# Optimization experiments

Hardware: AMD Instinct MI355X
Metric: run time of the kernel (lower is better)

The kernel has to match this reference:

```python
import jax, jax.numpy as jnp
import numpy as np

FEAT_STRIDE = 16
NMS_THRESH = 0.7
N_PRE = 6000    # eval-mode n_test_pre_nms
N_POST = 300    # eval-mode n_test_post_nms
MIN_SIZE = 16.0
NEG = -1e9
N_ANCHOR = 9


def generate_anchor_base():
    base = 16.0
    ratios = np.array([0.5, 1.0, 2.0], dtype=np.float64)
    scales = np.array([8.0, 16.0, 32.0], dtype=np.float64)
    h = (base * scales[None, :] * np.sqrt(ratios[:, None])).reshape(-1)
    w = (base * scales[None, :] * np.sqrt(1.0 / ratios[:, None])).reshape(-1)
    yc = xc = base / 2.0
    ab = np.stack([yc - h / 2, xc - w / 2, yc + h / 2, xc + w / 2], axis=1)
    return ab.astype(np.float32)  # [9,4] (y1,x1,y2,x2)


def enumerate_anchors(hh, ww):
    ab = generate_anchor_base()                       # [A,4]
    sy = np.arange(hh) * FEAT_STRIDE
    sx = np.arange(ww) * FEAT_STRIDE
    sx, sy = np.meshgrid(sx, sy)
    shift = np.stack([sy.ravel(), sx.ravel(), sy.ravel(), sx.ravel()], axis=1)  # [K,4]
    anchor = (shift[:, None, :] + ab[None, :, :]).reshape(-1, 4)                # [K*A,4]
    return jnp.asarray(anchor.astype(np.float32))


def conv2d(x, w, b, pad):
    y = jax.lax.conv_general_dilated(
        x, w, window_strides=(1, 1), padding=[(pad, pad), (pad, pad)],
        dimension_numbers=('NCHW', 'OIHW', 'NCHW'))
    return y + b[None, :, None, None]


def loc2bbox(anchor, loc):
    # anchor, loc: [K,4]; boxes as (y1,x1,y2,x2), deltas as (dy,dx,dh,dw)
    h = anchor[:, 2] - anchor[:, 0]
    w = anchor[:, 3] - anchor[:, 1]
    yc = anchor[:, 0] + 0.5 * h
    xc = anchor[:, 1] + 0.5 * w
    cy = loc[:, 0] * h + yc
    cx = loc[:, 1] * w + xc
    nh = jnp.exp(loc[:, 2]) * h
    nw = jnp.exp(loc[:, 3]) * w
    return jnp.stack([cy - 0.5 * nh, cx - 0.5 * nw, cy + 0.5 * nh, cx + 0.5 * nw], axis=1)


def iou_matrix(b):
    # b: [N,4] -> [N,N] pairwise IoU (same convention as torchvision.ops.nms)
    area = (b[:, 2] - b[:, 0]) * (b[:, 3] - b[:, 1])
    tl = jnp.maximum(b[:, None, :2], b[None, :, :2])
    br = jnp.minimum(b[:, None, 2:], b[None, :, 2:])
    wh = jnp.clip(br - tl, 0.0)
    inter = wh[..., 0] * wh[..., 1]
    return inter / (area[:, None] + area[None, :] - inter + 1e-9)


def propose(loc, score, anchor, img_h, img_w):
    # loc: [K,4] float, score: [K] fg prob, anchor: [K,4]
    roi = loc2bbox(anchor, loc)
    roi = jnp.stack([
        jnp.clip(roi[:, 0], 0.0, img_h), jnp.clip(roi[:, 1], 0.0, img_w),
        jnp.clip(roi[:, 2], 0.0, img_h), jnp.clip(roi[:, 3], 0.0, img_w)], axis=1)
    hs = roi[:, 2] - roi[:, 0]
    ws = roi[:, 3] - roi[:, 1]
    valid = (hs >= MIN_SIZE) & (ws >= MIN_SIZE)
    score = jnp.where(valid, score, NEG)        # filter-by-size via score masking
    vals, idx = jax.lax.top_k(score, N_PRE)      # descending score sort + pre-NMS cut
    boxes = roi[idx]                             # [N_PRE,4]
    iou = iou_matrix(boxes)
    supp0 = vals <= NEG / 2                      # filtered boxes start suppressed
    ar = jnp.arange(N_PRE)

    def body(i, supp):
        row = (iou[i] > NMS_THRESH) & (ar > i)
        return jnp.where(supp[i], supp, supp | row)

    supp = jax.lax.fori_loop(0, N_PRE, body, supp0)
    keep = ~supp
    kept = jnp.nonzero(keep, size=N_POST, fill_value=0)[0]
    n_keep = jnp.sum(keep)
    valid_out = jnp.arange(N_POST) < n_keep
    rois = jnp.where(valid_out[:, None], boxes[kept], 0.0)  # zero-padded [N_POST,4]
    return rois


def rpn_forward(x, conv1_w, conv1_b, score_w, score_b, loc_w, loc_b, img_h, img_w):
    n, _, hh, ww = x.shape
    anchor = enumerate_anchors(hh, ww)                        # [K*A,4]
    hidden = jax.nn.relu(conv2d(x, conv1_w, conv1_b, 1))      # [n,512,hh,ww]
    rpn_locs = conv2d(hidden, loc_w, loc_b, 0)                # [n,36,hh,ww]
    rpn_locs = rpn_locs.transpose(0, 2, 3, 1).reshape(n, -1, 4)
    raw = conv2d(hidden, score_w, score_b, 0).transpose(0, 2, 3, 1)  # [n,hh,ww,18]
    sm = jax.nn.softmax(raw.reshape(n, hh, ww, N_ANCHOR, 2), axis=4)
    fg = sm[..., 1].reshape(n, -1)                            # [n, K*A]
    rpn_scores = raw.reshape(n, -1, 2)
    rois = jax.vmap(lambda l, s: propose(l, s, anchor, float(img_h), float(img_w)))(rpn_locs, fg)
    roi_indices = jnp.repeat(jnp.arange(n, dtype=jnp.int32), N_POST)
    return rpn_locs, rpn_scores, rois.reshape(-1, 4), roi_indices, anchor


def setup_inputs() -> dict:
    key = jax.random.key(0)
    ks = jax.random.split(key, 7)
    n, c, hh, ww = 2, 512, 50, 84
    mid = 512
    x = jax.random.normal(ks[0], (n, c, hh, ww), dtype=jnp.float32)
    conv1_w = 0.01 * jax.random.normal(ks[1], (mid, c, 3, 3), dtype=jnp.float32)
    conv1_b = jnp.zeros((mid,), dtype=jnp.float32)
    score_w = 0.01 * jax.random.normal(ks[2], (N_ANCHOR * 2, mid, 1, 1), dtype=jnp.float32)
    score_b = jnp.zeros((N_ANCHOR * 2,), dtype=jnp.float32)
    loc_w = 0.01 * jax.random.normal(ks[3], (N_ANCHOR * 4, mid, 1, 1), dtype=jnp.float32)
    loc_b = jnp.zeros((N_ANCHOR * 4,), dtype=jnp.float32)
    return {"x": x, "conv1_w": conv1_w, "conv1_b": conv1_b,
            "score_w": score_w, "score_b": score_b,
            "loc_w": loc_w, "loc_b": loc_b,
            "img_h": 800, "img_w": 1344}


def reference(x, conv1_w, conv1_b, score_w, score_b, loc_w, loc_b, img_h, img_w):
    return rpn_forward(x, conv1_w, conv1_b, score_w, score_b, loc_w, loc_b, img_h, img_w)
```

## Files before the change

### kernel.cpp

```cpp
#include <hip/hip_runtime.h>
#include <hip/hip_bf16.h>
#include <math.h>

#define N_BATCH 2
#define HH 50
#define WW 84
#define NPIX (HH*WW)
#define KA (NPIX*9)
#define N_PRE 6000
#define N_POST 300
#define NMS_T 0.7f
#define NEGV (-1e9f)
#define NWORDS 94

#define OFF_LOCS   0
#define OFF_SCORES (N_BATCH*KA*4)
#define OFF_ROIS   (OFF_SCORES + N_BATCH*KA*2)
#define OFF_RIDX   (OFF_ROIS + N_BATCH*N_POST*4)
#define OFF_ANCH   (OFF_RIDX + N_BATCH*N_POST)

#define WS_HID    0ull
#define WS_ROI    17505600ull
#define WS_ITEMS  18715200ull
#define WS_SITEMS 19320000ull
#define WS_SBOX   19416000ull
#define WS_MASK   19608000ull
#define WS_DIAG   28632000ull
#define WS_HIST   28728000ull
#define WS_PEXT   28824000ull
#define WS_WT     WS_ITEMS
#define PART_BYTES 17203200ull

typedef unsigned long long u64;
typedef unsigned u32;

__global__ __launch_bounds__(64) void k_init(const float* __restrict__ w,
    float* __restrict__ wT3, u32* __restrict__ hists) {
  __shared__ float ls[64][19];
  const int t2 = blockIdx.x, ocb = blockIdx.y;
  const int tid = threadIdx.x;
  if (ocb == 8) {
    if (t2 == 0) for (int i = tid; i < 4 * 2 * 256; i += 64) hists[i] = 0;
    return;
  }
#pragma unroll
  for (int j = 0; j < 18; j++) {
    int idx = tid + j * 64;
    int oc = idx / 18, r = idx % 18;
    ls[oc][r] = w[(size_t)(ocb * 64 + oc) * 4608 + t2 * 18 + r];
  }
  __syncthreads();
  float* outp = wT3 + (size_t)(t2 * 8 + ocb) * 1152;
#pragma unroll
  for (int j = 0; j < 18; j++) {
    int idx = tid + j * 64;
    int q = idx / 64, oc = idx % 64;
    int kxky = q >> 1, icl = q & 1;
    int kx = kxky / 3, ky = kxky % 3;
    outp[idx] = ls[oc][icl * 9 + ky * 3 + kx];
  }
}

#define IC_T 2
__global__ __launch_bounds__(64, 2) void k_conv1(const float* __restrict__ x,
    const float* __restrict__ wT3,
    float* __restrict__ p0, float* __restrict__ p1,
    float* __restrict__ p2, float* __restrict__ p3,
    int ics_per) {
  const int ocb = blockIdx.x;
  const int row = blockIdx.y;
  const int icq = blockIdx.z >> 1;
  const int n   = blockIdx.z & 1;
  const int tid = threadIdx.x;
  const int g   = tid & 3;
  const int ocl = tid >> 2;
  const int ics0 = icq * ics_per;
  const int tiles = ics_per / IC_T;

  __shared__ __align__(16) float lx[IC_T * 3 * 96];

  const float* xg = x + ((size_t)n * 512 + ics0) * NPIX;

  int goff[9];
#pragma unroll
  for (int j = 0; j < 9; j++) {
    int idx = tid + j * 64;
    int ic = idx / 288; int rem = idx % 288;
    int rr = rem / 96;  int rem2 = rem % 96;
    int g2 = rem2 / 24; int q = rem2 % 24;
    int grow = row - 1 + rr;
    int gcol = g2 * 21 - 1 + q;
    bool v = ((unsigned)grow < 50u) && ((unsigned)gcol < 84u);
    goff[j] = v ? (ic * NPIX + grow * 84 + gcol) : -1;
  }

  float acc[4][21];
#pragma unroll
  for (int i = 0; i < 4; i++)
#pragma unroll
    for (int p = 0; p < 21; p++) acc[i][p] = 0.f;

  float xs[9];
  const float* wt = wT3 + ((size_t)(ics0 >> 1) * 8 + ocb) * 1152 + ocl * 4;
#pragma unroll
  for (int j = 0; j < 9; j++) xs[j] = (goff[j] >= 0) ? xg[goff[j]] : 0.f;

  for (int t = 0; t < tiles; t++) {
#pragma unroll
    for (int j = 0; j < 9; j++) lx[tid + j * 64] = xs[j];
    __syncthreads();

    if (t < tiles - 1) {
      int xadv = (t + 1) * IC_T * NPIX;
#pragma unroll
      for (int j = 0; j < 9; j++) xs[j] = (goff[j] >= 0) ? xg[goff[j] + xadv] : 0.f;
    }

#pragma unroll
    for (int icl = 0; icl < IC_T; icl++) {
#pragma unroll
      for (int ky = 0; ky < 3; ky++) {
        float xv[24];
        const float* lp = &lx[icl * 288 + ky * 96 + g * 24];
#pragma unroll
        for (int v4 = 0; v4 < 6; v4++) {
          float4 f = *(const float4*)&lp[v4 * 4];
          xv[v4 * 4 + 0] = f.x; xv[v4 * 4 + 1] = f.y;
          xv[v4 * 4 + 2] = f.z; xv[v4 * 4 + 3] = f.w;
        }
#pragma unroll
        for (int kx = 0; kx < 3; kx++) {
          float4 wv = *(const float4*)&wt[((kx * 3 + ky) * IC_T + icl) * 64];
          float wa[4] = {wv.x, wv.y, wv.z, wv.w};
#pragma unroll
          for (int i = 0; i < 4; i++)
#pragma unroll
            for (int p = 0; p < 21; p++)
              acc[i][p] = fmaf(wa[i], xv[p + kx], acc[i][p]);
        }
      }
    }
    __syncthreads();
    wt += 9216;
  }

  {
    float* hp = (icq == 0) ? p0 : (icq == 1) ? p1 : (icq == 2) ? p2 : p3;
    int oc = ocb * 64 + ocl * 4;
#pragma unroll
    for (int i = 0; i < 4; i++) {
      float* op = &hp[(size_t)(n * 512 + oc + i) * NPIX + row * 84 + g * 21];
#pragma unroll
      for (int p = 0; p < 21; p++) op[p] = acc[i][p];
    }
  }
}

__global__ __launch_bounds__(256) void k_head(
    const float* __restrict__ p0, const float* __restrict__ p1,
    const float* __restrict__ p2, const float* __restrict__ p3, int nsplit,
    const float* __restrict__ bias,
    const float* __restrict__ sw, const float* __restrict__ sb,
    const float* __restrict__ lww, const float* __restrict__ lb,
    const int* __restrict__ ihp, const int* __restrict__ iwp,
    float* __restrict__ out, float4* __restrict__ roi, u64* __restrict__ items) {
  const int tid = threadIdx.x;
  const int q = tid >> 6;
  const int pxl = tid & 63;
  const int P = blockIdx.x * 64 + pxl;
  const bool valid = P < N_BATCH * NPIX;
  const int n = P / NPIX, p = P - n * NPIX;
  const int o0 = q * 14;
  __shared__ float xt[32][64];
  __shared__ float wt[32][56];
  __shared__ float lall[64][57];

  float acc[14];
#pragma unroll
  for (int o = 0; o < 14; o++) acc[o] = 0.f;

  for (int c0 = 0; c0 < 512; c0 += 32) {
#pragma unroll
    for (int j = 0; j < 8; j++) {
      int idx = tid + j * 256;
      int c = idx >> 6, lp = idx & 63;
      int PP = blockIdx.x * 64 + lp;
      float v = 0.f;
      if (PP < N_BATCH * NPIX) {
        int nn = PP / NPIX, pp = PP - nn * NPIX;
        size_t off = (size_t)(nn * 512 + c0 + c) * NPIX + pp;
        v = p0[off];
        if (nsplit > 1) v += p1[off];
        if (nsplit > 2) { v += p2[off]; v += p3[off]; }
        v += bias[c0 + c];
        v = v > 0.f ? v : 0.f;
      }
      xt[c][lp] = v;
    }
    for (int i = tid; i < 32 * 54; i += 256) {
      int c = i / 54, o = i % 54;
      wt[c][o] = (o < 18) ? sw[o * 512 + c0 + c] : lww[(o - 18) * 512 + c0 + c];
    }
    __syncthreads();
#pragma unroll 4
    for (int c = 0; c < 32; c++) {
      float xv = xt[c][pxl];
      const float* wp = &wt[c][o0];
#pragma unroll
      for (int o = 0; o < 14; o++) acc[o] = fmaf(xv, wp[o], acc[o]);
    }
    __syncthreads();
  }

  if (valid) {
#pragma unroll
    for (int j = 0; j < 14; j++) {
      int o = o0 + j;
      if (o < 54) {
        float v = acc[j] + ((o < 18) ? sb[o] : lb[o - 18]);
        lall[pxl][o] = v;
        if (o < 18) out[OFF_SCORES + ((size_t)n * KA + (size_t)p * 9) * 2 + o] = v;
        else        out[OFF_LOCS + ((size_t)n * KA + (size_t)p * 9) * 4 + (o - 18)] = v;
      }
    }
  }
  __syncthreads();

  if (valid && q == 0) {
    const int pi = p / WW, pj = p - pi * WW;
    const float sy = (float)(pi * 16), sx = (float)(pj * 16);
    const float imh = (float)ihp[0], imw = (float)iwp[0];
#pragma unroll
    for (int a = 0; a < 9; a++) {
      int ri = a / 3, si = a % 3;
      double ratio = (ri == 0) ? 0.5 : ((ri == 1) ? 1.0 : 2.0);
      double scale = (si == 0) ? 8.0 : ((si == 1) ? 16.0 : 32.0);
      double hh = 16.0 * scale * sqrt(ratio);
      double ww = 16.0 * scale * sqrt(1.0 / ratio);
      float ay1 = (float)(8.0 - hh * 0.5), ax1 = (float)(8.0 - ww * 0.5);
      float ay2 = (float)(8.0 + hh * 0.5), ax2 = (float)(8.0 + ww * 0.5);
      float4 A = make_float4(sy + ay1, sx + ax1, sy + ay2, sx + ax2);
      int k = p * 9 + a;
      if (n == 0) ((float4*)out)[OFF_ANCH / 4 + k] = A;
      float r0 = lall[pxl][2 * a], r1 = lall[pxl][2 * a + 1];
      float m = fmaxf(r0, r1);
      float e0 = expf(r0 - m), e1 = expf(r1 - m);
      float fgv = e1 / (e0 + e1);
      float Lx = lall[pxl][18 + 4 * a],     Ly = lall[pxl][18 + 4 * a + 1];
      float Lz = lall[pxl][18 + 4 * a + 2], Lw = lall[pxl][18 + 4 * a + 3];
      float h = A.z - A.x, w = A.w - A.y;
      float yc = A.x + 0.5f * h, xc = A.y + 0.5f * w;
      float cy = Lx * h + yc, cx = Ly * w + xc;
      float nh = expf(Lz) * h, nw = expf(Lw) * w;
      float y1 = cy - 0.5f * nh, x1 = cx - 0.5f * nw;
      float y2 = cy + 0.5f * nh, x2 = cx + 0.5f * nw;
      y1 = fminf(fmaxf(y1, 0.f), imh); y2 = fminf(fmaxf(y2, 0.f), imh);
      x1 = fminf(fmaxf(x1, 0.f), imw); x2 = fminf(fmaxf(x2, 0.f), imw);
      bool ok = ((y2 - y1) >= 16.f) && ((x2 - x1) >= 16.f);
      float sc = ok ? fgv : NEGV;
      u32 u = __float_as_uint(sc);
      u32 key = (u & 0x80000000u) ? ~u : (u | 0x80000000u);
      roi[(size_t)n * KA + k] = make_float4(y1, x1, y2, x2);
      items[(size_t)n * KA + k] = ((u64)key << 32) | (u32)(~(u32)k);
    }
  }
}

__global__ __launch_bounds__(256) void k_pass(const u64* __restrict__ items,
    u32* __restrict__ hists, int p) {
  const int bx = blockIdx.x, b = blockIdx.y;
  const int tid = threadIdx.x;
  __shared__ u32 h8[8 * 256];
  __shared__ u32 lhist[256];
  __shared__ u32 shp[2];
  for (int i = tid; i < 2048; i += 256) h8[i] = 0;

  u32 prefix = 0, need = N_PRE;
  for (int q = 0; q < p; q++) {
    __syncthreads();
    for (int i = tid; i < 256; i += 256) lhist[i] = hists[(q * 2 + b) * 256 + i];
    __syncthreads();
    if (tid == 0) {
      u32 nd = need; int chosen = 0;
      for (int bb = 255; bb >= 0; bb--) {
        if (nd <= lhist[bb]) { chosen = bb; break; }
        nd -= lhist[bb];
      }
      shp[0] = (prefix << 8) | (u32)chosen; shp[1] = nd;
    }
    __syncthreads();
    prefix = shp[0]; need = shp[1];
  }
  __syncthreads();

  const u64* it = items + (size_t)b * KA;
  const int s = 3 - p;
  const int slice = tid & 7;
  for (int i = bx * 256 + tid; i < KA; i += 16 * 256) {
    u32 key = (u32)(it[i] >> 32);
    bool match = (p == 0) || ((key >> ((s + 1) * 8)) == prefix);
    if (match) atomicAdd(&h8[slice * 256 + ((key >> (s * 8)) & 255)], 1u);
  }
  __syncthreads();
  if (tid < 256) {
    u32 sum = 0;
#pragma unroll
    for (int k = 0; k < 8; k++) sum += h8[k * 256 + tid];
    if (sum) atomicAdd(&hists[(p * 2 + b) * 256 + tid], sum);
  }
}

__global__ __launch_bounds__(1024) void k_select2(const u64* __restrict__ items,
    const float4* __restrict__ roi, const u32* __restrict__ hists,
    u64* __restrict__ sitems, float4* __restrict__ sbox) {
  const int b = blockIdx.x;
  const int tid = threadIdx.x;
  const int lane = tid & 63;
  const u64* it = items + (size_t)b * KA;
  __shared__ u64 arr[8192];
  __shared__ u32 hist[256];
  __shared__ u32 sh_prefix, sh_need, sh_cnt;
  if (tid == 0) sh_cnt = 0;

  u32 prefix = 0, need = N_PRE;
  for (int q = 0; q < 4; q++) {
    __syncthreads();
    for (int i = tid; i < 256; i += 1024) hist[i] = hists[(q * 2 + b) * 256 + i];
    __syncthreads();
    if (tid == 0) {
      u32 nd = need; int chosen = 0;
      for (int bb = 255; bb >= 0; bb--) {
        if (nd <= hist[bb]) { chosen = bb; break; }
        nd -= hist[bb];
      }
      sh_prefix = (prefix << 8) | (u32)chosen; sh_need = nd;
    }
    __syncthreads();
    prefix = sh_prefix; need = sh_need;
  }
  u32 kth = prefix;
  __syncthreads();

  for (int i0 = 0; i0 < KA; i0 += 1024) {
    int i = i0 + tid;
    u64 v = (i < KA) ? it[i] : 0ull;
    bool sel = (i < KA) && ((u32)(v >> 32) >= kth);
    u64 bal = __ballot(sel);
    u32 cnt = (u32)__popcll(bal);
    u32 base = 0;
    if (lane == 0 && cnt) base = atomicAdd(&sh_cnt, cnt);
    base = (u32)__shfl((int)base, 0, 64);
    if (sel) {
      u32 pos = base + (u32)__popcll(bal & ((1ull << lane) - 1ull));
      if (pos < 8192) arr[pos] = v;
    }
  }
  __syncthreads();
  u32 T = sh_cnt; if (T > 8192) T = 8192;
  for (int i = (int)T + tid; i < 8192; i += 1024) arr[i] = 0ull;

  for (u32 k = 2; k <= 8192; k <<= 1) {
    for (u32 j = k >> 1; j > 0; j >>= 1) {
      __syncthreads();
#pragma unroll 4
      for (u32 m = tid; m < 4096; m += 1024) {
        u32 mm = m & (j - 1);
        u32 i = ((m - mm) << 1) + mm;
        u32 l = i + j;
        u64 a = arr[i], c = arr[l];
        bool dir = ((i & k) == 0);
        if ((a < c) == dir) { arr[i] = c; arr[l] = a; }
      }
    }
  }
  __syncthreads();
  for (int i = tid; i < N_PRE; i += 1024) {
    u64 v = arr[i];
    sitems[(size_t)b * N_PRE + i] = v;
    u32 kk = ~(u32)(v & 0xffffffffull);
    float4 bx = make_float4(0, 0, 0, 0);
    if (kk < KA) bx = roi[(size_t)b * KA + kk];
    sbox[(size_t)b * N_PRE + i] = bx;
  }
}

__global__ __launch_bounds__(64) void k_mask(const float4* __restrict__ sbox,
    u64* __restrict__ mask, u64* __restrict__ diag) {
  const int cb = blockIdx.x, rb = blockIdx.y, b = blockIdx.z;
  if (cb < rb) return;
  const int tid = threadIdx.x;
  __shared__ float4 cbx[64];
  __shared__ float carea[64];
  int col0 = cb * 64;
  int c = col0 + tid;
  float4 v = (c < N_PRE) ? sbox[(size_t)b * N_PRE + c] : make_float4(0, 0, 0, 0);
  cbx[tid] = v;
  carea[tid] = (v.z - v.x) * (v.w - v.y);
  __syncthreads();
  int row = rb * 64 + tid;
  if (row >= N_PRE) return;
  float4 r = sbox[(size_t)b * N_PRE + row];
  float rarea = (r.z - r.x) * (r.w - r.y);
  u64 word = 0ull;
  for (int j = 0; j < 64; j++) {
    int cc = col0 + j;
    if (cc > row && cc < N_PRE) {
      float4 q = cbx[j];
      float ty = fmaxf(r.x, q.x), tx = fmaxf(r.y, q.y);
      float by = fminf(r.z, q.z), bx = fminf(r.w, q.w);
      float ihh = fmaxf(by - ty, 0.f), iww = fmaxf(bx - tx, 0.f);
      float inter = ihh * iww;
      float iou = inter / (rarea + carea[j] - inter + 1e-9f);
      if (iou > NMS_T) word |= (1ull << j);
    }
  }
  mask[((size_t)b * N_PRE + row) * NWORDS + cb] = word;
  if (cb == rb) diag[(size_t)b * N_PRE + row] = word;
}

__global__ __launch_bounds__(64) void k_nms_out(const u64* __restrict__ sitems,
    const float4* __restrict__ sbox, const u64* __restrict__ mask,
    const u64* __restrict__ diag, float* __restrict__ out) {
  const int b = blockIdx.x;
  const int lane = threadIdx.x;
  __shared__ u64 remv[NWORDS];
  __shared__ u64 pre[NWORDS];
  __shared__ u64 dia[N_PRE];
  __shared__ u32 keep[N_POST];
  for (int i = lane; i < NWORDS; i += 64) { remv[i] = 0ull; pre[i] = 0ull; }
  __syncthreads();
  u32 keyneg = ~__float_as_uint(NEGV);
  for (int i = lane; i < N_PRE; i += 64) {
    dia[i] = diag[(size_t)b * N_PRE + i];
    u32 key = (u32)(sitems[(size_t)b * N_PRE + i] >> 32);
    if (key == keyneg || key == 0u)
      atomicOr(&pre[i >> 6], 1ull << (i & 63));
  }
  if (lane == 0) pre[NWORDS - 1] |= ~((1ull << (N_PRE - 64 * (NWORDS - 1))) - 1ull);
  __syncthreads();

  int kc = 0;
  for (int g = 0; g < NWORDS && kc < N_POST; g++) {
    u64 done = 0ull;
    while (kc < N_POST) {
      u64 cur = remv[g] | pre[g] | done;
      if (cur == ~0ull) break;
      int r0 = -1, r1 = -1, r2 = -1, r3 = -1; int m = 1;
      u64 c2 = cur;
      int bit = __ffsll((long long)(~c2)) - 1;
      r0 = g * 64 + bit; c2 |= (1ull << bit) | dia[r0]; done |= 1ull << bit;
      if (c2 != ~0ull && kc + 1 < N_POST) {
        bit = __ffsll((long long)(~c2)) - 1;
        r1 = g * 64 + bit; c2 |= (1ull << bit) | dia[r1]; done |= 1ull << bit; m = 2;
        if (c2 != ~0ull && kc + 2 < N_POST) {
          bit = __ffsll((long long)(~c2)) - 1;
          r2 = g * 64 + bit; c2 |= (1ull << bit) | dia[r2]; done |= 1ull << bit; m = 3;
          if (c2 != ~0ull && kc + 3 < N_POST) {
            bit = __ffsll((long long)(~c2)) - 1;
            r3 = g * 64 + bit; c2 |= (1ull << bit) | dia[r3]; done |= 1ull << bit; m = 4;
          }
        }
      }
      if (lane == 0) {
        keep[kc] = (u32)r0;
        if (m > 1) keep[kc + 1] = (u32)r1;
        if (m > 2) keep[kc + 2] = (u32)r2;
        if (m > 3) keep[kc + 3] = (u32)r3;
      }
      int j = lane >> 4, l16 = lane & 15;
      int rj = (j == 0) ? r0 : (j == 1) ? r1 : (j == 2) ? r2 : r3;
      if (j < m) {
        const u64* mrow = mask + ((size_t)b * N_PRE + rj) * NWORDS;
        for (int cb = g + l16; cb < NWORDS; cb += 16)
          atomicOr(&remv[cb], mrow[cb]);
      }
      kc += m;
      __syncthreads();
    }
  }
  __syncthreads();
  for (int r = lane; r < N_POST; r += 64) {
    float4 bx = make_float4(0, 0, 0, 0);
    if (r < kc) bx = sbox[(size_t)b * N_PRE + keep[r]];
    ((float4*)out)[OFF_ROIS / 4 + (size_t)b * N_POST + r] = bx;
    out[OFF_RIDX + (size_t)b * N_POST + r] = (float)b;
  }
}

extern "C" void kernel_launch(void* const* d_in, const int* in_sizes, int n_in,
                              void* d_out, int out_size, void* d_ws, size_t ws_size,
                              hipStream_t stream) {
  const float* x   = (const float*)d_in[0];
  const float* c1w = (const float*)d_in[1];
  const float* c1b = (const float*)d_in[2];
  const float* sw  = (const float*)d_in[3];
  const float* sb  = (const float*)d_in[4];
  const float* lw  = (const float*)d_in[5];
  const float* lb  = (const float*)d_in[6];
  const int* ih    = (const int*)d_in[7];
  const int* iw    = (const int*)d_in[8];
  float* out = (float*)d_out;
  char* wsb = (char*)d_ws;

  float* hid   = (float*)(wsb + WS_HID);
  float4* roi  = (float4*)(wsb + WS_ROI);
  u64* items   = (u64*)(wsb + WS_ITEMS);
  u64* sitems  = (u64*)(wsb + WS_SITEMS);
  float4* sbox = (float4*)(wsb + WS_SBOX);
  u64* maskp   = (u64*)(wsb + WS_MASK);
  u64* diagp   = (u64*)(wsb + WS_DIAG);
  u32* hists   = (u32*)(wsb + WS_HIST);
  float* wT3   = (float*)(wsb + WS_WT);

  int nsplit = 1;
  if (ws_size >= WS_PEXT + 3 * PART_BYTES) nsplit = 4;
  else if (ws_size >= WS_PEXT + 1 * PART_BYTES) nsplit = 2;
  float* p1 = (nsplit > 1) ? (float*)(wsb + WS_PEXT) : hid;
  float* p2 = (nsplit > 2) ? (float*)(wsb + WS_PEXT + PART_BYTES) : hid;
  float* p3 = (nsplit > 2) ? (float*)(wsb + WS_PEXT + 2 * PART_BYTES) : hid;

  hipLaunchKernelGGL(k_init, dim3(256, 9), dim3(64), 0, stream, c1w, wT3, hists);
  hipLaunchKernelGGL(k_conv1, dim3(8, 50, 2 * nsplit), dim3(64), 0, stream,
                     x, wT3, hid, p1, p2, p3, 512 / nsplit);
  hipLaunchKernelGGL(k_head, dim3(132), dim3(256), 0, stream,
                     hid, p1, p2, p3, nsplit, c1b, sw, sb, lw, lb, ih, iw,
                     out, roi, items);
  for (int p = 0; p < 4; p++)
    hipLaunchKernelGGL(k_pass, dim3(16, 2), dim3(256), 0, stream, items, hists, p);
  hipLaunchKernelGGL(k_select2, dim3(2), dim3(1024), 0, stream,
                     items, roi, hists, sitems, sbox);
  hipLaunchKernelGGL(k_mask, dim3(NWORDS, NWORDS, 2), dim3(64), 0, stream, sbox, maskp, diagp);
  hipLaunchKernelGGL(k_nms_out, dim3(2), dim3(64), 0, stream, sitems, sbox, maskp, diagp, out);
}
```

Baseline: 1.127 ms.

## Double-buffer conv1 input and weight tiles in LDS via global_load_lds

```diff
diff --git a/kernel.cpp b/kernel.cpp
--- a/kernel.cpp
+++ b/kernel.cpp
@@ -27,6 +27,7 @@
 #define WS_MASK   19608000ull
 #define WS_DIAG   28632000ull
 #define WS_HIST   28728000ull
+#define WS_ZERO   28736192ull
 #define WS_PEXT   28824000ull
 #define WS_WT     WS_ITEMS
 #define PART_BYTES 17203200ull
@@ -34,13 +35,19 @@
 typedef unsigned long long u64;
 typedef unsigned u32;
 
+#define AS1 __attribute__((address_space(1)))
+#define AS3 __attribute__((address_space(3)))
+
 __global__ __launch_bounds__(64) void k_init(const float* __restrict__ w,
-    float* __restrict__ wT3, u32* __restrict__ hists) {
+    float* __restrict__ wT3, u32* __restrict__ hists, float* __restrict__ zbuf) {
   __shared__ float ls[64][19];
   const int t2 = blockIdx.x, ocb = blockIdx.y;
   const int tid = threadIdx.x;
   if (ocb == 8) {
-    if (t2 == 0) for (int i = tid; i < 4 * 2 * 256; i += 64) hists[i] = 0;
+    if (t2 == 0) {
+      for (int i = tid; i < 4 * 2 * 256; i += 64) hists[i] = 0;
+      if (tid < 64) zbuf[tid] = 0.f;
+    }
     return;
   }
 #pragma unroll
@@ -63,7 +70,7 @@
 
 #define IC_T 2
 __global__ __launch_bounds__(64, 2) void k_conv1(const float* __restrict__ x,
-    const float* __restrict__ wT3,
+    const float* __restrict__ wT3, const float* __restrict__ zsrc,
     float* __restrict__ p0, float* __restrict__ p1,
     float* __restrict__ p2, float* __restrict__ p3,
     int ics_per) {
@@ -77,7 +84,8 @@
   const int ics0 = icq * ics_per;
   const int tiles = ics_per / IC_T;
 
-  __shared__ __align__(16) float lx[IC_T * 3 * 96];
+  __shared__ __align__(16) float lx[2][IC_T * 3 * 96];
+  __shared__ __align__(16) float lw[2][IC_T * 9 * 64];
 
   const float* xg = x + ((size_t)n * 512 + ics0) * NPIX;
 
@@ -100,20 +108,36 @@
 #pragma unroll
     for (int p = 0; p < 21; p++) acc[i][p] = 0.f;
 
-  float xs[9];
-  const float* wt = wT3 + ((size_t)(ics0 >> 1) * 8 + ocb) * 1152 + ocl * 4;
-#pragma unroll
-  for (int j = 0; j < 9; j++) xs[j] = (goff[j] >= 0) ? xg[goff[j]] : 0.f;
+  const float* wt0 = wT3 + ((size_t)(ics0 >> 1) * 8 + ocb) * 1152 + tid;
+
+#pragma unroll
+  for (int j = 0; j < 9; j++) {
+    const float* gp = (goff[j] >= 0) ? (xg + goff[j]) : zsrc;
+    __builtin_amdgcn_global_load_lds((const AS1 void*)gp,
+                                     (AS3 void*)&lx[0][j * 64], 4, 0, 0);
+  }
+#pragma unroll
+  for (int j = 0; j < 18; j++)
+    __builtin_amdgcn_global_load_lds((const AS1 void*)(wt0 + j * 64),
+                                     (AS3 void*)&lw[0][j * 64], 4, 0, 0);
 
   for (int t = 0; t < tiles; t++) {
-#pragma unroll
-    for (int j = 0; j < 9; j++) lx[tid + j * 64] = xs[j];
-    __syncthreads();
-
-    if (t < tiles - 1) {
-      int xadv = (t + 1) * IC_T * NPIX;
-#pragma unroll
-      for (int j = 0; j < 9; j++) xs[j] = (goff[j] >= 0) ? xg[goff[j] + xadv] : 0.f;
+    const int cur = t & 1;
+    asm volatile("s_waitcnt vmcnt(0)" ::: "memory");
+    if (t + 1 < tiles) {
+      const int nxt = cur ^ 1;
+      const int xadv = (t + 1) * IC_T * NPIX;
+      const float* wtn = wt0 + (size_t)(t + 1) * 9216;
+#pragma unroll
+      for (int j = 0; j < 9; j++) {
+        const float* gp = (goff[j] >= 0) ? (xg + goff[j] + xadv) : zsrc;
+        __builtin_amdgcn_global_load_lds((const AS1 void*)gp,
+                                         (AS3 void*)&lx[nxt][j * 64], 4, 0, 0);
+      }
+#pragma unroll
+      for (int j = 0; j < 18; j++)
+        __builtin_amdgcn_global_load_lds((const AS1 void*)(wtn + j * 64),
+                                         (AS3 void*)&lw[nxt][j * 64], 4, 0, 0);
     }
 
 #pragma unroll
@@ -121,7 +145,7 @@
 #pragma unroll
       for (int ky = 0; ky < 3; ky++) {
         float xv[24];
-        const float* lp = &lx[icl * 288 + ky * 96 + g * 24];
+        const float* lp = &lx[cur][icl * 288 + ky * 96 + g * 24];
 #pragma unroll
         for (int v4 = 0; v4 < 6; v4++) {
           float4 f = *(const float4*)&lp[v4 * 4];
@@ -130,7 +154,7 @@
         }
 #pragma unroll
         for (int kx = 0; kx < 3; kx++) {
-          float4 wv = *(const float4*)&wt[((kx * 3 + ky) * IC_T + icl) * 64];
+          float4 wv = *(const float4*)&lw[cur][((kx * 3 + ky) * IC_T + icl) * 64 + ocl * 4];
           float wa[4] = {wv.x, wv.y, wv.z, wv.w};
 #pragma unroll
           for (int i = 0; i < 4; i++)
@@ -140,8 +164,6 @@
         }
       }
     }
-    __syncthreads();
-    wt += 9216;
   }
 
   {
@@ -510,6 +532,7 @@
   u64* maskp   = (u64*)(wsb + WS_MASK);
   u64* diagp   = (u64*)(wsb + WS_DIAG);
   u32* hists   = (u32*)(wsb + WS_HIST);
+  float* zbuf  = (float*)(wsb + WS_ZERO);
   float* wT3   = (float*)(wsb + WS_WT);
 
   int nsplit = 1;
@@ -519,9 +542,9 @@
   float* p2 = (nsplit > 2) ? (float*)(wsb + WS_PEXT + PART_BYTES) : hid;
   float* p3 = (nsplit > 2) ? (float*)(wsb + WS_PEXT + 2 * PART_BYTES) : hid;
 
-  hipLaunchKernelGGL(k_init, dim3(256, 9), dim3(64), 0, stream, c1w, wT3, hists);
+  hipLaunchKernelGGL(k_init, dim3(256, 9), dim3(64), 0, stream, c1w, wT3, hists, zbuf);
   hipLaunchKernelGGL(k_conv1, dim3(8, 50, 2 * nsplit), dim3(64), 0, stream,
-                     x, wT3, hid, p1, p2, p3, 512 / nsplit);
+                     x, wT3, zbuf, hid, p1, p2, p3, 512 / nsplit);
   hipLaunchKernelGGL(k_head, dim3(132), dim3(256), 0, stream,
                      hid, p1, p2, p3, nsplit, c1b, sw, sb, lw, lb, ih, iw,
                      out, roi, items);
```

Result: no change. 1.108 ms (-1.6%).
